# Kernel optimization log

Measured on AMD Instinct MI355X. Metric: run time of the kernel, lower is better.

## Reference

```python
import jax, jax.numpy as jnp
import numpy as np
from jax import lax

T, B, S, D, V = 128, 512, 128, 128, 50257


def setup_inputs() -> dict:
    key = jax.random.key(0)
    ks = jax.random.split(key, 6)
    words = jax.random.randint(ks[0], (T, B), 0, V, dtype=jnp.int64)
    masks = jnp.ones((T, B), dtype=jnp.float32)
    tparams = jax.random.normal(ks[1], (S, S), dtype=jnp.float32)
    tag_embed = jax.random.normal(ks[2], (S, D), dtype=jnp.float32)
    word_embed = jax.random.normal(ks[3], (V, D), dtype=jnp.float32)
    transform = jax.random.normal(ks[4], (D, D), dtype=jnp.float32) * 0.05 + jnp.eye(D, dtype=jnp.float32)
    correction = jax.random.normal(ks[5], (S, V), dtype=jnp.float32) * 0.05
    return {"words": words, "masks": masks, "tparams": tparams,
            "tag_embed": tag_embed, "word_embed": word_embed,
            "transform": transform, "correction": correction}


def reference(words, masks, tparams, tag_embed, word_embed, transform, correction):
    num_state = tparams.shape[0]
    # update_emission (unsupervised mode): project word embeddings, score against tags,
    # add correction, log_softmax over the vocab dimension (dim=0 of (V,S)).
    word_emb = word_embed @ transform                      # (V, D)
    log_emission = jax.nn.log_softmax(word_emb @ tag_embed.T + correction.T, axis=0)  # (V, S)
    # _calc_logA: log-normalized transition matrix (rows = source state)
    logA = jax.nn.log_softmax(tparams, axis=1)             # (S, S)
    # uniform log prior pi = log(1/S)
    log_pi = jnp.full((num_state,), jnp.log(1.0 / num_state), dtype=log_emission.dtype)

    em = log_emission[words]                               # (T, B, S) gathered densities

    alpha0 = log_pi[None, :] + em[0]                       # (B, S)

    def step(alpha, inp):
        dens, m = inp                                      # (B,S), (B,)
        # _forward_cell: logsumexp over previous state of alpha + logA + density
        new = jax.nn.logsumexp(alpha[:, :, None] + logA[None, :, :] + dens[:, None, :], axis=1)
        m = m[:, None]
        alpha = m * new + (1.0 - m) * alpha
        return alpha, None

    alpha, _ = lax.scan(step, alpha0, (em[1:], masks[1:]))
    objective = jnp.sum(jax.nn.logsumexp(alpha, axis=1))
    return -objective
```

## Files before the change

kernel.cpp:

```cpp
#include <hip/hip_runtime.h>
#include <math.h>

#define T_ 128
#define B_ 512
#define S_ 128
#define D_ 128
#define V_ 50257

#define K2_VT 64
#define K2_NB ((V_ + K2_VT - 1) / K2_VT)

__global__ __launch_bounds__(128) void k1_m2(const float* __restrict__ transform,
                                             const float* __restrict__ tag_embed,
                                             float* __restrict__ M2) {
  __shared__ float te[128][129];
  int tid = threadIdx.x;
  for (int r = 0; r < 128; ++r) te[r][tid] = tag_embed[r * 128 + tid];
  __syncthreads();
  int k = blockIdx.x;
  float acc = 0.f;
  #pragma unroll 8
  for (int d = 0; d < 128; ++d) acc += transform[k * 128 + d] * te[tid][d];
  M2[k * 128 + tid] = acc;
}

__global__ __launch_bounds__(64) void k1b_a(const float* __restrict__ tparams,
                                            float* __restrict__ A) {
  int i = blockIdx.x;
  int l = threadIdx.x;
  float x0 = tparams[i * 128 + l];
  float x1 = tparams[i * 128 + 64 + l];
  float m = fmaxf(x0, x1);
  #pragma unroll
  for (int off = 32; off; off >>= 1) m = fmaxf(m, __shfl_xor(m, off));
  float e0 = __expf(x0 - m), e1 = __expf(x1 - m);
  float s = e0 + e1;
  #pragma unroll
  for (int off = 32; off; off >>= 1) s += __shfl_xor(s, off);
  float inv = 1.f / s;
  A[i * 128 + l]      = e0 * inv;
  A[i * 128 + 64 + l] = e1 * inv;
}

__global__ __launch_bounds__(256, 2) void k2_logits(const float* __restrict__ we,
                                                 const float* __restrict__ M2,
                                                 const float* __restrict__ corr,
                                                 float* __restrict__ logits,
                                                 float* __restrict__ pmaxb,
                                                 float* __restrict__ psumb) {
  int tid = threadIdx.x;
  int sc = tid & 31;
  int vg = tid >> 5;
  long v0 = (long)blockIdx.x * K2_VT;
  __shared__ float weT[128][68];
  __shared__ float m2t[64][128];

  #pragma unroll
  for (int it = 0; it < 32; ++it) {
    int idx = it * 256 + tid;
    int d = idx & 127;
    int vv = idx >> 7;
    long v = v0 + vv;
    weT[d][vv] = (v < V_) ? we[v * 128 + d] : 0.f;
  }

  float acc[8][4];
  #pragma unroll
  for (int u = 0; u < 8; ++u)
    #pragma unroll
    for (int e = 0; e < 4; ++e) acc[u][e] = 0.f;

  #pragma unroll
  for (int c = 0; c < 2; ++c) {
    __syncthreads();
    #pragma unroll
    for (int it = 0; it < 32; ++it) {
      int idx = it * 256 + tid;
      int kr = idx >> 7, s = idx & 127;
      m2t[kr][s] = M2[(c * 64 + kr) * 128 + s];
    }
    __syncthreads();
    #pragma unroll 8
    for (int k = 0; k < 64; ++k) {
      float4 mv = *(const float4*)&m2t[k][4 * sc];
      float4 w0 = *(const float4*)&weT[c * 64 + k][8 * vg];
      float4 w1 = *(const float4*)&weT[c * 64 + k][8 * vg + 4];
      acc[0][0] += w0.x * mv.x; acc[0][1] += w0.x * mv.y; acc[0][2] += w0.x * mv.z; acc[0][3] += w0.x * mv.w;
      acc[1][0] += w0.y * mv.x; acc[1][1] += w0.y * mv.y; acc[1][2] += w0.y * mv.z; acc[1][3] += w0.y * mv.w;
      acc[2][0] += w0.z * mv.x; acc[2][1] += w0.z * mv.y; acc[2][2] += w0.z * mv.z; acc[2][3] += w0.z * mv.w;
      acc[3][0] += w0.w * mv.x; acc[3][1] += w0.w * mv.y; acc[3][2] += w0.w * mv.z; acc[3][3] += w0.w * mv.w;
      acc[4][0] += w1.x * mv.x; acc[4][1] += w1.x * mv.y; acc[4][2] += w1.x * mv.z; acc[4][3] += w1.x * mv.w;
      acc[5][0] += w1.y * mv.x; acc[5][1] += w1.y * mv.y; acc[5][2] += w1.y * mv.z; acc[5][3] += w1.y * mv.w;
      acc[6][0] += w1.z * mv.x; acc[6][1] += w1.z * mv.y; acc[6][2] += w1.z * mv.z; acc[6][3] += w1.z * mv.w;
      acc[7][0] += w1.w * mv.x; acc[7][1] += w1.w * mv.y; acc[7][2] += w1.w * mv.z; acc[7][3] += w1.w * mv.w;
    }
  }

  float lm[4], ls[4], Lst[8][4];
  #pragma unroll
  for (int e = 0; e < 4; ++e) { lm[e] = -INFINITY; ls[e] = 0.f; }
  long vbase = v0 + 8 * vg;
  #pragma unroll
  for (int e = 0; e < 4; ++e) {
    long rbase = (long)(4 * sc + e) * V_ + vbase;
    #pragma unroll
    for (int u = 0; u < 8; ++u) {
      if (vbase + u < V_) {
        float L = acc[u][e] + corr[rbase + u];
        Lst[u][e] = L;
        float nm = fmaxf(lm[e], L);
        ls[e] = ls[e] * __expf(lm[e] - nm) + __expf(L - nm);
        lm[e] = nm;
      }
    }
  }
  #pragma unroll
  for (int u = 0; u < 8; ++u) {
    long v = vbase + u;
    if (v < V_) {
      float4 st = make_float4(Lst[u][0], Lst[u][1], Lst[u][2], Lst[u][3]);
      *(float4*)&logits[v * 128 + 4 * sc] = st;
    }
  }

  __syncthreads();
  float* pmx = (float*)m2t;
  float* psm = pmx + 8 * 128;
  #pragma unroll
  for (int e = 0; e < 4; ++e) {
    pmx[vg * 128 + 4 * sc + e] = lm[e];
    psm[vg * 128 + 4 * sc + e] = ls[e];
  }
  __syncthreads();
  if (tid < 128) {
    int s = tid;
    float m = -INFINITY, sum = 0.f;
    #pragma unroll
    for (int g = 0; g < 8; ++g) {
      float pm = pmx[g * 128 + s];
      if (pm > -1e30f) {
        float ps = psm[g * 128 + s];
        float nm = fmaxf(m, pm);
        sum = sum * __expf(m - nm) + ps * __expf(pm - nm);
        m = nm;
      }
    }
    pmaxb[blockIdx.x * 128 + s] = m;
    psumb[blockIdx.x * 128 + s] = sum;
  }
}

__global__ __launch_bounds__(256) void k3_c(const float* __restrict__ pmaxb,
                                            const float* __restrict__ psumb,
                                            float* __restrict__ C) {
  int s = blockIdx.x;
  int t = threadIdx.x;
  float m = -INFINITY, sum = 0.f;
  #pragma unroll
  for (int q = 0; q < 4; ++q) {
    int b = t + q * 256;
    if (b < K2_NB) {
      float pm = pmaxb[b * 128 + s];
      if (pm > -1e30f) {
        float ps = psumb[b * 128 + s];
        float nm = fmaxf(m, pm);
        sum = sum * __expf(m - nm) + ps * __expf(pm - nm);
        m = nm;
      }
    }
  }
  #pragma unroll
  for (int off = 32; off; off >>= 1) {
    float om = __shfl_xor(m, off);
    float os = __shfl_xor(sum, off);
    float nm = fmaxf(m, om);
    sum = sum * __expf(m - nm) + os * __expf(om - nm);
    m = nm;
  }
  __shared__ float wm[4], wsv[4];
  int lane = t & 63, wv = t >> 6;
  if (lane == 0) { wm[wv] = m; wsv[wv] = sum; }
  __syncthreads();
  if (t == 0) {
    float M = fmaxf(fmaxf(wm[0], wm[1]), fmaxf(wm[2], wm[3]));
    float S = wsv[0] * __expf(wm[0] - M) + wsv[1] * __expf(wm[1] - M)
            + wsv[2] * __expf(wm[2] - M) + wsv[3] * __expf(wm[3] - M);
    C[s] = M + __logf(S);
  }
}

__global__ __launch_bounds__(512, 4) void k4_rec(const int* __restrict__ words,
                                              const float* __restrict__ masks,
                                              const float* __restrict__ A,
                                              const float* __restrict__ C,
                                              const float* __restrict__ logits,
                                              float* __restrict__ bv) {
  const float kB = 70.70101247f;
  int tid = threadIdx.x;
  int j = tid & 127;
  int h = tid >> 7;
  int b = blockIdx.x;
  int lane = tid & 63, w = tid >> 6;
  __shared__ __align__(16) float els[128];
  __shared__ __align__(16) float part[128][4];
  __shared__ __align__(16) float pmax4[4];
  __shared__ float wred[2];
  __shared__ int   wbuf[128];
  __shared__ float mbuf[128];
  if (tid < 128) {
    wbuf[j] = words[j * B_ + b];
    mbuf[j] = masks[j * B_ + b];
  }
  float Ac[32];
  #pragma unroll
  for (int k = 0; k < 32; ++k) Ac[k] = A[(h * 32 + k) * 128 + j];
  __syncthreads();

  float a = 0.f, S = 0.f, em_cur = 0.f, Lnext = 0.f, Cj = 0.f, a0 = 0.f;
  if (tid < 128) {
    Cj = C[j];
    a0 = -4.852030263919617f + logits[(unsigned)(wbuf[0] * 128 + j)] - Cj;
    float wm = a0;
    #pragma unroll
    for (int off = 32; off; off >>= 1) wm = fmaxf(wm, __shfl_xor(wm, off));
    if (lane == 0) wred[w] = wm;
  }
  __syncthreads();
  if (tid < 128) {
    float M0 = fmaxf(wred[0], wred[1]);
    a = __expf(a0 - M0);
    S = M0;
    els[j] = a;
    float L1 = logits[(unsigned)(wbuf[1] * 128 + j)];
    Lnext    = logits[(unsigned)(wbuf[2] * 128 + j)];
    em_cur = __expf(L1 - Cj + kB);
  }
  __syncthreads();

  for (int t = 1; t < T_; ++t) {
    float4 e0 = ((const float4*)els)[h * 8 + 0];
    float4 e1 = ((const float4*)els)[h * 8 + 1];
    float4 e2 = ((const float4*)els)[h * 8 + 2];
    float4 e3 = ((const float4*)els)[h * 8 + 3];
    float4 e4 = ((const float4*)els)[h * 8 + 4];
    float4 e5 = ((const float4*)els)[h * 8 + 5];
    float4 e6 = ((const float4*)els)[h * 8 + 6];
    float4 e7 = ((const float4*)els)[h * 8 + 7];
    float p0 = e0.x * Ac[0]  + e0.y * Ac[1]  + e0.z * Ac[2]  + e0.w * Ac[3]
             + e1.x * Ac[4]  + e1.y * Ac[5]  + e1.z * Ac[6]  + e1.w * Ac[7];
    float p1 = e2.x * Ac[8]  + e2.y * Ac[9]  + e2.z * Ac[10] + e2.w * Ac[11]
             + e3.x * Ac[12] + e3.y * Ac[13] + e3.z * Ac[14] + e3.w * Ac[15];
    float p2 = e4.x * Ac[16] + e4.y * Ac[17] + e4.z * Ac[18] + e4.w * Ac[19]
             + e5.x * Ac[20] + e5.y * Ac[21] + e5.z * Ac[22] + e5.w * Ac[23];
    float p3 = e6.x * Ac[24] + e6.y * Ac[25] + e6.z * Ac[26] + e6.w * Ac[27]
             + e7.x * Ac[28] + e7.y * Ac[29] + e7.z * Ac[30] + e7.w * Ac[31];
    part[j][h] = (p0 + p1) + (p2 + p3);
    if (j == 0) {
      float4 ma = make_float4(fmaxf(e0.x, e1.x), fmaxf(e0.y, e1.y), fmaxf(e0.z, e1.z), fmaxf(e0.w, e1.w));
      float4 mb = make_float4(fmaxf(e2.x, e3.x), fmaxf(e2.y, e3.y), fmaxf(e2.z, e3.z), fmaxf(e2.w, e3.w));
      float4 mc = make_float4(fmaxf(e4.x, e5.x), fmaxf(e4.y, e5.y), fmaxf(e4.z, e5.z), fmaxf(e4.w, e5.w));
      float4 md = make_float4(fmaxf(e6.x, e7.x), fmaxf(e6.y, e7.y), fmaxf(e6.z, e7.z), fmaxf(e6.w, e7.w));
      float4 m1 = make_float4(fmaxf(ma.x, mb.x), fmaxf(ma.y, mb.y), fmaxf(ma.z, mb.z), fmaxf(ma.w, mb.w));
      float4 m2 = make_float4(fmaxf(mc.x, md.x), fmaxf(mc.y, md.y), fmaxf(mc.z, md.z), fmaxf(mc.w, md.w));
      float mx = fmaxf(fmaxf(fmaxf(m1.x, m1.y), fmaxf(m1.z, m1.w)),
                       fmaxf(fmaxf(m2.x, m2.y), fmaxf(m2.z, m2.w)));
      pmax4[h] = mx;
    }
    float em_next = 0.f, Lf = 0.f;
    if (tid < 128) {
      if (t + 2 < T_) Lf = logits[(unsigned)(wbuf[t + 2] * 128 + j)];
      em_next = __expf(Lnext - Cj + kB);
    }
    __syncthreads();
    if (tid < 128) {
      float4 pm4 = *(const float4*)pmax4;
      float Mst = fmaxf(fmaxf(pm4.x, pm4.y), fmaxf(pm4.z, pm4.w));
      float invM = 1.f / Mst;
      float4 pp = *(const float4*)&part[j][0];
      float P = (pp.x + pp.y) + (pp.z + pp.w);
      float nv   = (P * invM) * em_cur;
      float oldq = (a * invM) * 0x1p102f;
      float mm = mbuf[t];
      a = mm * nv + (1.f - mm) * oldq;
      els[j] = a;
      S += __logf(Mst) - kB;
      em_cur = em_next;
      Lnext = Lf;
    }
    __syncthreads();
  }

  if (tid < 128) {
    float ss = a;
    #pragma unroll
    for (int off = 32; off; off >>= 1) ss += __shfl_xor(ss, off);
    if (lane == 0) wred[w] = ss;
  }
  __syncthreads();
  if (tid == 0) bv[b] = S + __logf(wred[0] + wred[1]);
}

__global__ __launch_bounds__(256) void k5_sum(const float* __restrict__ bv,
                                              float* __restrict__ out) {
  int t = threadIdx.x;
  float s = bv[t] + bv[t + 256];
  #pragma unroll
  for (int off = 32; off; off >>= 1) s += __shfl_xor(s, off);
  __shared__ float wsm[4];
  if ((t & 63) == 0) wsm[t >> 6] = s;
  __syncthreads();
  if (t == 0) out[0] = -(wsm[0] + wsm[1] + wsm[2] + wsm[3]);
}

extern "C" void kernel_launch(void* const* d_in, const int* in_sizes, int n_in,
                              void* d_out, int out_size, void* d_ws, size_t ws_size,
                              hipStream_t stream) {
  const int*   words      = (const int*)d_in[0];
  const float* masks      = (const float*)d_in[1];
  const float* tparams    = (const float*)d_in[2];
  const float* tag_embed  = (const float*)d_in[3];
  const float* word_embed = (const float*)d_in[4];
  const float* transform  = (const float*)d_in[5];
  const float* correction = (const float*)d_in[6];

  float* ws     = (float*)d_ws;
  float* M2     = ws;
  float* A      = ws + 16384;
  float* C      = ws + 32768;
  float* bv     = ws + 32896;
  float* pmaxb  = ws + 33408;
  float* psumb  = ws + 134016;
  float* logits = ws + 234624;

  hipLaunchKernelGGL(k1_m2,    dim3(128),    dim3(128), 0, stream, transform, tag_embed, M2);
  hipLaunchKernelGGL(k1b_a,    dim3(128),    dim3(64),  0, stream, tparams, A);
  hipLaunchKernelGGL(k2_logits,dim3(K2_NB),  dim3(256), 0, stream, word_embed, M2, correction, logits, pmaxb, psumb);
  hipLaunchKernelGGL(k3_c,     dim3(S_),     dim3(256), 0, stream, pmaxb, psumb, C);
  hipLaunchKernelGGL(k4_rec,   dim3(512),    dim3(512), 0, stream, words, masks, A, C, logits, bv);
  hipLaunchKernelGGL(k5_sum,   dim3(1),      dim3(256), 0, stream, bv, (float*)d_out);
}
```

Before: 193.4 us.

## Run recurrence with one wavefront per batch, holding full transition matrix in registers

The forward recurrence kernel now uses a single 64-lane wavefront per batch element instead of 512 threads. Each lane owns two states and keeps their full 128-entry columns of the transition matrix in registers. The per-step dot products, max and sum reductions are done with in-wave shuffles, so both block-wide barriers per time step go away. The cost is roughly eight times more FMAs per lane per step, very heavy register pressure with a possible spill, and only about two waves per CU to hide latency.

```diff
diff --git a/kernel.cpp b/kernel.cpp
--- a/kernel.cpp
+++ b/kernel.cpp
@@ -189,115 +189,112 @@
   }
 }
 
-__global__ __launch_bounds__(512, 4) void k4_rec(const int* __restrict__ words,
-                                              const float* __restrict__ masks,
-                                              const float* __restrict__ A,
-                                              const float* __restrict__ C,
-                                              const float* __restrict__ logits,
-                                              float* __restrict__ bv) {
+#define CHAIN8(EA, EB, AC, B) \
+  (EA.x * AC[B] + EA.y * AC[(B)+1] + EA.z * AC[(B)+2] + EA.w * AC[(B)+3] + \
+   EB.x * AC[(B)+4] + EB.y * AC[(B)+5] + EB.z * AC[(B)+6] + EB.w * AC[(B)+7])
+
+#define DOT_H(H, G0, G1) { \
+  float4 x0 = ELS4[(H)*8+0]; float4 x1 = ELS4[(H)*8+1]; \
+  float4 x2 = ELS4[(H)*8+2]; float4 x3 = ELS4[(H)*8+3]; \
+  float4 x4 = ELS4[(H)*8+4]; float4 x5 = ELS4[(H)*8+5]; \
+  float4 x6 = ELS4[(H)*8+6]; float4 x7 = ELS4[(H)*8+7]; \
+  float p00 = CHAIN8(x0, x1, Ac0, (H)*32+0); \
+  float p01 = CHAIN8(x2, x3, Ac0, (H)*32+8); \
+  float p02 = CHAIN8(x4, x5, Ac0, (H)*32+16); \
+  float p03 = CHAIN8(x6, x7, Ac0, (H)*32+24); \
+  float p10 = CHAIN8(x0, x1, Ac1, (H)*32+0); \
+  float p11 = CHAIN8(x2, x3, Ac1, (H)*32+8); \
+  float p12 = CHAIN8(x4, x5, Ac1, (H)*32+16); \
+  float p13 = CHAIN8(x6, x7, Ac1, (H)*32+24); \
+  G0 = (p00 + p01) + (p02 + p03); \
+  G1 = (p10 + p11) + (p12 + p13); }
+
+__global__ __launch_bounds__(64, 1) void k4_rec(const int* __restrict__ words,
+                                                const float* __restrict__ masks,
+                                                const float* __restrict__ A,
+                                                const float* __restrict__ C,
+                                                const float* __restrict__ logits,
+                                                float* __restrict__ bv) {
   const float kB = 70.70101247f;
-  int tid = threadIdx.x;
-  int j = tid & 127;
-  int h = tid >> 7;
+  int l = threadIdx.x;
   int b = blockIdx.x;
-  int lane = tid & 63, w = tid >> 6;
   __shared__ __align__(16) float els[128];
-  __shared__ __align__(16) float part[128][4];
-  __shared__ __align__(16) float pmax4[4];
-  __shared__ float wred[2];
   __shared__ int   wbuf[128];
   __shared__ float mbuf[128];
-  if (tid < 128) {
-    wbuf[j] = words[j * B_ + b];
-    mbuf[j] = masks[j * B_ + b];
-  }
-  float Ac[32];
-  #pragma unroll
-  for (int k = 0; k < 32; ++k) Ac[k] = A[(h * 32 + k) * 128 + j];
-  __syncthreads();
-
-  float a = 0.f, S = 0.f, em_cur = 0.f, Lnext = 0.f, Cj = 0.f, a0 = 0.f;
-  if (tid < 128) {
-    Cj = C[j];
-    a0 = -4.852030263919617f + logits[(unsigned)(wbuf[0] * 128 + j)] - Cj;
-    float wm = a0;
-    #pragma unroll
-    for (int off = 32; off; off >>= 1) wm = fmaxf(wm, __shfl_xor(wm, off));
-    if (lane == 0) wred[w] = wm;
-  }
-  __syncthreads();
-  if (tid < 128) {
-    float M0 = fmaxf(wred[0], wred[1]);
-    a = __expf(a0 - M0);
-    S = M0;
-    els[j] = a;
-    float L1 = logits[(unsigned)(wbuf[1] * 128 + j)];
-    Lnext    = logits[(unsigned)(wbuf[2] * 128 + j)];
-    em_cur = __expf(L1 - Cj + kB);
-  }
-  __syncthreads();
+  wbuf[l]      = words[l * B_ + b];
+  wbuf[l + 64] = words[(l + 64) * B_ + b];
+  mbuf[l]      = masks[l * B_ + b];
+  mbuf[l + 64] = masks[(l + 64) * B_ + b];
+
+  float Ac0[128], Ac1[128];
+  #pragma unroll
+  for (int i = 0; i < 128; ++i) {
+    Ac0[i] = A[i * 128 + l];
+    Ac1[i] = A[i * 128 + 64 + l];
+  }
+  float Cj0 = C[l], Cj1 = C[l + 64];
+  __syncthreads();
+
+  int w0 = wbuf[0];
+  float a0i = -4.852030263919617f + logits[(unsigned)(w0 * 128 + l)] - Cj0;
+  float a1i = -4.852030263919617f + logits[(unsigned)(w0 * 128 + 64 + l)] - Cj1;
+  float m0 = a0i, m1 = a1i;
+  #pragma unroll
+  for (int off = 32; off; off >>= 1) {
+    m0 = fmaxf(m0, __shfl_xor(m0, off));
+    m1 = fmaxf(m1, __shfl_xor(m1, off));
+  }
+  float M0 = fmaxf(m0, m1);
+  float a0 = __expf(a0i - M0), a1 = __expf(a1i - M0);
+  float S = M0;
+  els[l] = a0; els[l + 64] = a1;
+  float Mst = fmaxf(a0, a1);
+  #pragma unroll
+  for (int off = 32; off; off >>= 1) Mst = fmaxf(Mst, __shfl_xor(Mst, off));
+  int w1 = wbuf[1];
+  float Lc0 = logits[(unsigned)(w1 * 128 + l)];
+  float Lc1 = logits[(unsigned)(w1 * 128 + 64 + l)];
+
+  const float4* ELS4 = (const float4*)els;
 
   for (int t = 1; t < T_; ++t) {
-    float4 e0 = ((const float4*)els)[h * 8 + 0];
-    float4 e1 = ((const float4*)els)[h * 8 + 1];
-    float4 e2 = ((const float4*)els)[h * 8 + 2];
-    float4 e3 = ((const float4*)els)[h * 8 + 3];
-    float4 e4 = ((const float4*)els)[h * 8 + 4];
-    float4 e5 = ((const float4*)els)[h * 8 + 5];
-    float4 e6 = ((const float4*)els)[h * 8 + 6];
-    float4 e7 = ((const float4*)els)[h * 8 + 7];
-    float p0 = e0.x * Ac[0]  + e0.y * Ac[1]  + e0.z * Ac[2]  + e0.w * Ac[3]
-             + e1.x * Ac[4]  + e1.y * Ac[5]  + e1.z * Ac[6]  + e1.w * Ac[7];
-    float p1 = e2.x * Ac[8]  + e2.y * Ac[9]  + e2.z * Ac[10] + e2.w * Ac[11]
-             + e3.x * Ac[12] + e3.y * Ac[13] + e3.z * Ac[14] + e3.w * Ac[15];
-    float p2 = e4.x * Ac[16] + e4.y * Ac[17] + e4.z * Ac[18] + e4.w * Ac[19]
-             + e5.x * Ac[20] + e5.y * Ac[21] + e5.z * Ac[22] + e5.w * Ac[23];
-    float p3 = e6.x * Ac[24] + e6.y * Ac[25] + e6.z * Ac[26] + e6.w * Ac[27]
-             + e7.x * Ac[28] + e7.y * Ac[29] + e7.z * Ac[30] + e7.w * Ac[31];
-    part[j][h] = (p0 + p1) + (p2 + p3);
-    if (j == 0) {
-      float4 ma = make_float4(fmaxf(e0.x, e1.x), fmaxf(e0.y, e1.y), fmaxf(e0.z, e1.z), fmaxf(e0.w, e1.w));
-      float4 mb = make_float4(fmaxf(e2.x, e3.x), fmaxf(e2.y, e3.y), fmaxf(e2.z, e3.z), fmaxf(e2.w, e3.w));
-      float4 mc = make_float4(fmaxf(e4.x, e5.x), fmaxf(e4.y, e5.y), fmaxf(e4.z, e5.z), fmaxf(e4.w, e5.w));
-      float4 md = make_float4(fmaxf(e6.x, e7.x), fmaxf(e6.y, e7.y), fmaxf(e6.z, e7.z), fmaxf(e6.w, e7.w));
-      float4 m1 = make_float4(fmaxf(ma.x, mb.x), fmaxf(ma.y, mb.y), fmaxf(ma.z, mb.z), fmaxf(ma.w, mb.w));
-      float4 m2 = make_float4(fmaxf(mc.x, md.x), fmaxf(mc.y, md.y), fmaxf(mc.z, md.z), fmaxf(mc.w, md.w));
-      float mx = fmaxf(fmaxf(fmaxf(m1.x, m1.y), fmaxf(m1.z, m1.w)),
-                       fmaxf(fmaxf(m2.x, m2.y), fmaxf(m2.z, m2.w)));
-      pmax4[h] = mx;
-    }
-    float em_next = 0.f, Lf = 0.f;
-    if (tid < 128) {
-      if (t + 2 < T_) Lf = logits[(unsigned)(wbuf[t + 2] * 128 + j)];
-      em_next = __expf(Lnext - Cj + kB);
-    }
-    __syncthreads();
-    if (tid < 128) {
-      float4 pm4 = *(const float4*)pmax4;
-      float Mst = fmaxf(fmaxf(pm4.x, pm4.y), fmaxf(pm4.z, pm4.w));
-      float invM = 1.f / Mst;
-      float4 pp = *(const float4*)&part[j][0];
-      float P = (pp.x + pp.y) + (pp.z + pp.w);
-      float nv   = (P * invM) * em_cur;
-      float oldq = (a * invM) * 0x1p102f;
-      float mm = mbuf[t];
-      a = mm * nv + (1.f - mm) * oldq;
-      els[j] = a;
-      S += __logf(Mst) - kB;
-      em_cur = em_next;
-      Lnext = Lf;
-    }
-    __syncthreads();
-  }
-
-  if (tid < 128) {
-    float ss = a;
-    #pragma unroll
-    for (int off = 32; off; off >>= 1) ss += __shfl_xor(ss, off);
-    if (lane == 0) wred[w] = ss;
-  }
-  __syncthreads();
-  if (tid == 0) bv[b] = S + __logf(wred[0] + wred[1]);
+    int wn = wbuf[(t < T_ - 1) ? (t + 1) : t];
+    float Lp0 = logits[(unsigned)(wn * 128 + l)];
+    float Lp1 = logits[(unsigned)(wn * 128 + 64 + l)];
+
+    float G00, G01, G02, G03, G10, G11, G12, G13;
+    DOT_H(0, G00, G10)
+    DOT_H(1, G01, G11)
+    DOT_H(2, G02, G12)
+    DOT_H(3, G03, G13)
+    float P0 = (G00 + G01) + (G02 + G03);
+    float P1 = (G10 + G11) + (G12 + G13);
+
+    float em0 = __expf(Lc0 - Cj0 + kB);
+    float em1 = __expf(Lc1 - Cj1 + kB);
+    float invM = 1.f / Mst;
+    float mm = mbuf[t];
+    float nv0 = (P0 * invM) * em0;
+    float nv1 = (P1 * invM) * em1;
+    float oldq0 = (a0 * invM) * 0x1p102f;
+    float oldq1 = (a1 * invM) * 0x1p102f;
+    a0 = mm * nv0 + (1.f - mm) * oldq0;
+    a1 = mm * nv1 + (1.f - mm) * oldq1;
+    els[l] = a0; els[l + 64] = a1;
+    S += __logf(Mst) - kB;
+    Mst = fmaxf(a0, a1);
+    #pragma unroll
+    for (int off = 32; off; off >>= 1) Mst = fmaxf(Mst, __shfl_xor(Mst, off));
+    Lc0 = Lp0; Lc1 = Lp1;
+  }
+
+  float s0 = a0, s1 = a1;
+  #pragma unroll
+  for (int off = 32; off; off >>= 1) {
+    s0 += __shfl_xor(s0, off);
+    s1 += __shfl_xor(s1, off);
+  }
+  if (l == 0) bv[b] = S + __logf(s0 + s1);
 }
 
 __global__ __launch_bounds__(256) void k5_sum(const float* __restrict__ bv,
@@ -336,6 +333,6 @@
   hipLaunchKernelGGL(k1b_a,    dim3(128),    dim3(64),  0, stream, tparams, A);
   hipLaunchKernelGGL(k2_logits,dim3(K2_NB),  dim3(256), 0, stream, word_embed, M2, correction, logits, pmaxb, psumb);
   hipLaunchKernelGGL(k3_c,     dim3(S_),     dim3(256), 0, stream, pmaxb, psumb, C);
-  hipLaunchKernelGGL(k4_rec,   dim3(512),    dim3(512), 0, stream, words, masks, A, C, logits, bv);
+  hipLaunchKernelGGL(k4_rec,   dim3(512),    dim3(64),  0, stream, words, masks, A, C, logits, bv);
   hipLaunchKernelGGL(k5_sum,   dim3(1),      dim3(256), 0, stream, bv, (float*)d_out);
 }
```

New measurement: 210.0 us. 8.6% more time.

## Process two batch sequences per block in forward recurrence to reuse transition registers

Applied to the files above, without the earlier changes.

The forward-recurrence kernel now handles two batch elements per block instead of one. Each thread applies its 32 register-resident transition coefficients to both sequences' alpha vectors, and twice as many threads take part in the elementwise update. The grid halves to 256 blocks, which spreads the per-step barrier and A-load cost over more work. In exchange register pressure rises (launch bounds lowered to 2 blocks per CU) and fewer blocks are in flight across the device.

```diff
diff --git a/kernel.cpp b/kernel.cpp
--- a/kernel.cpp
+++ b/kernel.cpp
@@ -189,100 +189,116 @@
   }
 }
 
-__global__ __launch_bounds__(512, 4) void k4_rec(const int* __restrict__ words,
-                                              const float* __restrict__ masks,
-                                              const float* __restrict__ A,
-                                              const float* __restrict__ C,
-                                              const float* __restrict__ logits,
-                                              float* __restrict__ bv) {
+#define CHAIN8(EA, EB, AC, BASE) \
+  (EA.x * AC[(BASE)]   + EA.y * AC[(BASE)+1] + EA.z * AC[(BASE)+2] + EA.w * AC[(BASE)+3] + \
+   EB.x * AC[(BASE)+4] + EB.y * AC[(BASE)+5] + EB.z * AC[(BASE)+6] + EB.w * AC[(BASE)+7])
+
+#define SLICEMAX8(E0,E1,E2,E3,E4,E5,E6,E7, OUT) { \
+  float4 ma = make_float4(fmaxf(E0.x,E1.x), fmaxf(E0.y,E1.y), fmaxf(E0.z,E1.z), fmaxf(E0.w,E1.w)); \
+  float4 mb = make_float4(fmaxf(E2.x,E3.x), fmaxf(E2.y,E3.y), fmaxf(E2.z,E3.z), fmaxf(E2.w,E3.w)); \
+  float4 mc = make_float4(fmaxf(E4.x,E5.x), fmaxf(E4.y,E5.y), fmaxf(E4.z,E5.z), fmaxf(E4.w,E5.w)); \
+  float4 md = make_float4(fmaxf(E6.x,E7.x), fmaxf(E6.y,E7.y), fmaxf(E6.z,E7.z), fmaxf(E6.w,E7.w)); \
+  float4 m1 = make_float4(fmaxf(ma.x,mb.x), fmaxf(ma.y,mb.y), fmaxf(ma.z,mb.z), fmaxf(ma.w,mb.w)); \
+  float4 m2 = make_float4(fmaxf(mc.x,md.x), fmaxf(mc.y,md.y), fmaxf(mc.z,md.z), fmaxf(mc.w,md.w)); \
+  OUT = fmaxf(fmaxf(fmaxf(m1.x,m1.y), fmaxf(m1.z,m1.w)), \
+              fmaxf(fmaxf(m2.x,m2.y), fmaxf(m2.z,m2.w))); }
+
+__global__ __launch_bounds__(512, 2) void k4_rec(const int* __restrict__ words,
+                                                 const float* __restrict__ masks,
+                                                 const float* __restrict__ A,
+                                                 const float* __restrict__ C,
+                                                 const float* __restrict__ logits,
+                                                 float* __restrict__ bv) {
   const float kB = 70.70101247f;
   int tid = threadIdx.x;
   int j = tid & 127;
   int h = tid >> 7;
-  int b = blockIdx.x;
-  int lane = tid & 63, w = tid >> 6;
-  __shared__ __align__(16) float els[128];
-  __shared__ __align__(16) float part[128][4];
-  __shared__ __align__(16) float pmax4[4];
-  __shared__ float wred[2];
-  __shared__ int   wbuf[128];
-  __shared__ float mbuf[128];
-  if (tid < 128) {
-    wbuf[j] = words[j * B_ + b];
-    mbuf[j] = masks[j * B_ + b];
+  int b0 = blockIdx.x * 2;
+  int lane = tid & 63;
+  __shared__ __align__(16) float els[2][128];
+  __shared__ float part[2][4][128];
+  __shared__ __align__(16) float pmax[2][4];
+  __shared__ float sred[2][2];
+  __shared__ int   wbuf[2][128];
+  __shared__ float mbuf[2][128];
+
+  if (tid < 256) {
+    int gg = tid >> 7, t0 = tid & 127;
+    wbuf[gg][t0] = words[t0 * B_ + b0 + gg];
+    mbuf[gg][t0] = masks[t0 * B_ + b0 + gg];
   }
   float Ac[32];
   #pragma unroll
   for (int k = 0; k < 32; ++k) Ac[k] = A[(h * 32 + k) * 128 + j];
   __syncthreads();
 
-  float a = 0.f, S = 0.f, em_cur = 0.f, Lnext = 0.f, Cj = 0.f, a0 = 0.f;
-  if (tid < 128) {
+  int g = (tid >> 7) & 1;
+  float a = 0.f, S = 0.f, em_cur = 0.f, Lnext = 0.f, Cj = 0.f, a0i = 0.f;
+  if (tid < 256) {
     Cj = C[j];
-    a0 = -4.852030263919617f + logits[(unsigned)(wbuf[0] * 128 + j)] - Cj;
-    float wm = a0;
+    a0i = -4.852030263919617f + logits[(unsigned)(wbuf[g][0] * 128 + j)] - Cj;
+    float wm = a0i;
     #pragma unroll
     for (int off = 32; off; off >>= 1) wm = fmaxf(wm, __shfl_xor(wm, off));
-    if (lane == 0) wred[w] = wm;
-  }
-  __syncthreads();
-  if (tid < 128) {
-    float M0 = fmaxf(wred[0], wred[1]);
-    a = __expf(a0 - M0);
+    if (lane == 0) sred[g][(tid >> 6) & 1] = wm;
+  }
+  __syncthreads();
+  if (tid < 256) {
+    float M0 = fmaxf(sred[g][0], sred[g][1]);
+    a = __expf(a0i - M0);
     S = M0;
-    els[j] = a;
-    float L1 = logits[(unsigned)(wbuf[1] * 128 + j)];
-    Lnext    = logits[(unsigned)(wbuf[2] * 128 + j)];
+    els[g][j] = a;
+    float L1 = logits[(unsigned)(wbuf[g][1] * 128 + j)];
+    Lnext    = logits[(unsigned)(wbuf[g][2] * 128 + j)];
     em_cur = __expf(L1 - Cj + kB);
   }
   __syncthreads();
 
+  const float4* E0 = (const float4*)&els[0][0];
+  const float4* E1 = (const float4*)&els[1][0];
+
   for (int t = 1; t < T_; ++t) {
-    float4 e0 = ((const float4*)els)[h * 8 + 0];
-    float4 e1 = ((const float4*)els)[h * 8 + 1];
-    float4 e2 = ((const float4*)els)[h * 8 + 2];
-    float4 e3 = ((const float4*)els)[h * 8 + 3];
-    float4 e4 = ((const float4*)els)[h * 8 + 4];
-    float4 e5 = ((const float4*)els)[h * 8 + 5];
-    float4 e6 = ((const float4*)els)[h * 8 + 6];
-    float4 e7 = ((const float4*)els)[h * 8 + 7];
-    float p0 = e0.x * Ac[0]  + e0.y * Ac[1]  + e0.z * Ac[2]  + e0.w * Ac[3]
-             + e1.x * Ac[4]  + e1.y * Ac[5]  + e1.z * Ac[6]  + e1.w * Ac[7];
-    float p1 = e2.x * Ac[8]  + e2.y * Ac[9]  + e2.z * Ac[10] + e2.w * Ac[11]
-             + e3.x * Ac[12] + e3.y * Ac[13] + e3.z * Ac[14] + e3.w * Ac[15];
-    float p2 = e4.x * Ac[16] + e4.y * Ac[17] + e4.z * Ac[18] + e4.w * Ac[19]
-             + e5.x * Ac[20] + e5.y * Ac[21] + e5.z * Ac[22] + e5.w * Ac[23];
-    float p3 = e6.x * Ac[24] + e6.y * Ac[25] + e6.z * Ac[26] + e6.w * Ac[27]
-             + e7.x * Ac[28] + e7.y * Ac[29] + e7.z * Ac[30] + e7.w * Ac[31];
-    part[j][h] = (p0 + p1) + (p2 + p3);
+    float4 x0 = E0[h * 8 + 0], x1 = E0[h * 8 + 1], x2 = E0[h * 8 + 2], x3 = E0[h * 8 + 3];
+    float4 x4 = E0[h * 8 + 4], x5 = E0[h * 8 + 5], x6 = E0[h * 8 + 6], x7 = E0[h * 8 + 7];
+    float4 y0 = E1[h * 8 + 0], y1 = E1[h * 8 + 1], y2 = E1[h * 8 + 2], y3 = E1[h * 8 + 3];
+    float4 y4 = E1[h * 8 + 4], y5 = E1[h * 8 + 5], y6 = E1[h * 8 + 6], y7 = E1[h * 8 + 7];
+    {
+      float p0 = CHAIN8(x0, x1, Ac, 0);
+      float p1 = CHAIN8(x2, x3, Ac, 8);
+      float p2 = CHAIN8(x4, x5, Ac, 16);
+      float p3 = CHAIN8(x6, x7, Ac, 24);
+      part[0][h][j] = (p0 + p1) + (p2 + p3);
+    }
+    {
+      float p0 = CHAIN8(y0, y1, Ac, 0);
+      float p1 = CHAIN8(y2, y3, Ac, 8);
+      float p2 = CHAIN8(y4, y5, Ac, 16);
+      float p3 = CHAIN8(y6, y7, Ac, 24);
+      part[1][h][j] = (p0 + p1) + (p2 + p3);
+    }
     if (j == 0) {
-      float4 ma = make_float4(fmaxf(e0.x, e1.x), fmaxf(e0.y, e1.y), fmaxf(e0.z, e1.z), fmaxf(e0.w, e1.w));
-      float4 mb = make_float4(fmaxf(e2.x, e3.x), fmaxf(e2.y, e3.y), fmaxf(e2.z, e3.z), fmaxf(e2.w, e3.w));
-      float4 mc = make_float4(fmaxf(e4.x, e5.x), fmaxf(e4.y, e5.y), fmaxf(e4.z, e5.z), fmaxf(e4.w, e5.w));
-      float4 md = make_float4(fmaxf(e6.x, e7.x), fmaxf(e6.y, e7.y), fmaxf(e6.z, e7.z), fmaxf(e6.w, e7.w));
-      float4 m1 = make_float4(fmaxf(ma.x, mb.x), fmaxf(ma.y, mb.y), fmaxf(ma.z, mb.z), fmaxf(ma.w, mb.w));
-      float4 m2 = make_float4(fmaxf(mc.x, md.x), fmaxf(mc.y, md.y), fmaxf(mc.z, md.z), fmaxf(mc.w, md.w));
-      float mx = fmaxf(fmaxf(fmaxf(m1.x, m1.y), fmaxf(m1.z, m1.w)),
-                       fmaxf(fmaxf(m2.x, m2.y), fmaxf(m2.z, m2.w)));
-      pmax4[h] = mx;
+      float mx0, mx1;
+      SLICEMAX8(x0, x1, x2, x3, x4, x5, x6, x7, mx0)
+      SLICEMAX8(y0, y1, y2, y3, y4, y5, y6, y7, mx1)
+      pmax[0][h] = mx0;
+      pmax[1][h] = mx1;
     }
     float em_next = 0.f, Lf = 0.f;
-    if (tid < 128) {
-      if (t + 2 < T_) Lf = logits[(unsigned)(wbuf[t + 2] * 128 + j)];
+    if (tid < 256) {
+      if (t + 2 < T_) Lf = logits[(unsigned)(wbuf[g][t + 2] * 128 + j)];
       em_next = __expf(Lnext - Cj + kB);
     }
     __syncthreads();
-    if (tid < 128) {
-      float4 pm4 = *(const float4*)pmax4;
+    if (tid < 256) {
+      float4 pm4 = *(const float4*)pmax[g];
       float Mst = fmaxf(fmaxf(pm4.x, pm4.y), fmaxf(pm4.z, pm4.w));
       float invM = 1.f / Mst;
-      float4 pp = *(const float4*)&part[j][0];
-      float P = (pp.x + pp.y) + (pp.z + pp.w);
+      float P = (part[g][0][j] + part[g][1][j]) + (part[g][2][j] + part[g][3][j]);
       float nv   = (P * invM) * em_cur;
       float oldq = (a * invM) * 0x1p102f;
-      float mm = mbuf[t];
+      float mm = mbuf[g][t];
       a = mm * nv + (1.f - mm) * oldq;
-      els[j] = a;
+      els[g][j] = a;
       S += __logf(Mst) - kB;
       em_cur = em_next;
       Lnext = Lf;
@@ -290,14 +306,15 @@
     __syncthreads();
   }
 
-  if (tid < 128) {
+  if (tid < 256) {
     float ss = a;
     #pragma unroll
     for (int off = 32; off; off >>= 1) ss += __shfl_xor(ss, off);
-    if (lane == 0) wred[w] = ss;
-  }
-  __syncthreads();
-  if (tid == 0) bv[b] = S + __logf(wred[0] + wred[1]);
+    if (lane == 0) sred[g][(tid >> 6) & 1] = ss;
+  }
+  __syncthreads();
+  if (tid == 0)   bv[b0]     = S + __logf(sred[0][0] + sred[0][1]);
+  if (tid == 128) bv[b0 + 1] = S + __logf(sred[1][0] + sred[1][1]);
 }
 
 __global__ __launch_bounds__(256) void k5_sum(const float* __restrict__ bv,
@@ -336,6 +353,6 @@
   hipLaunchKernelGGL(k1b_a,    dim3(128),    dim3(64),  0, stream, tparams, A);
   hipLaunchKernelGGL(k2_logits,dim3(K2_NB),  dim3(256), 0, stream, word_embed, M2, correction, logits, pmaxb, psumb);
   hipLaunchKernelGGL(k3_c,     dim3(S_),     dim3(256), 0, stream, pmaxb, psumb, C);
-  hipLaunchKernelGGL(k4_rec,   dim3(512),    dim3(512), 0, stream, words, masks, A, C, logits, bv);
+  hipLaunchKernelGGL(k4_rec,   dim3(256),    dim3(512), 0, stream, words, masks, A, C, logits, bv);
   hipLaunchKernelGGL(k5_sum,   dim3(1),      dim3(256), 0, stream, bv, (float*)d_out);
 }
```

New measurement: 194.6 us. About the same (+0.6%).

## Stream word embeddings directly from global in logits GEMM, transpose partial-sum buffer

Applied to the files above, without the earlier changes.

The logits kernel no longer stages a transposed word-embedding tile in shared memory. Each thread now loads its eight embedding rows straight from global memory as float4 per k-chunk. This frees shared memory, so the occupancy hint rises from 2 to 4 blocks per CU, and the M2 tile is loaded with float4 copies. In the recurrence kernel the partial-sum buffer becomes [4][128] to avoid strided LDS writes, at the cost of four scalar reads instead of one float4 read.

```diff
diff --git a/kernel.cpp b/kernel.cpp
--- a/kernel.cpp
+++ b/kernel.cpp
@@ -42,7 +42,18 @@
   A[i * 128 + 64 + l] = e1 * inv;
 }
 
-__global__ __launch_bounds__(256, 2) void k2_logits(const float* __restrict__ we,
+#define K2STEP(COMP, KK) { \
+  float4 mv = *(const float4*)&m2t[(KK)][4 * sc]; \
+  acc[0][0] += wr[0].COMP * mv.x; acc[0][1] += wr[0].COMP * mv.y; acc[0][2] += wr[0].COMP * mv.z; acc[0][3] += wr[0].COMP * mv.w; \
+  acc[1][0] += wr[1].COMP * mv.x; acc[1][1] += wr[1].COMP * mv.y; acc[1][2] += wr[1].COMP * mv.z; acc[1][3] += wr[1].COMP * mv.w; \
+  acc[2][0] += wr[2].COMP * mv.x; acc[2][1] += wr[2].COMP * mv.y; acc[2][2] += wr[2].COMP * mv.z; acc[2][3] += wr[2].COMP * mv.w; \
+  acc[3][0] += wr[3].COMP * mv.x; acc[3][1] += wr[3].COMP * mv.y; acc[3][2] += wr[3].COMP * mv.z; acc[3][3] += wr[3].COMP * mv.w; \
+  acc[4][0] += wr[4].COMP * mv.x; acc[4][1] += wr[4].COMP * mv.y; acc[4][2] += wr[4].COMP * mv.z; acc[4][3] += wr[4].COMP * mv.w; \
+  acc[5][0] += wr[5].COMP * mv.x; acc[5][1] += wr[5].COMP * mv.y; acc[5][2] += wr[5].COMP * mv.z; acc[5][3] += wr[5].COMP * mv.w; \
+  acc[6][0] += wr[6].COMP * mv.x; acc[6][1] += wr[6].COMP * mv.y; acc[6][2] += wr[6].COMP * mv.z; acc[6][3] += wr[6].COMP * mv.w; \
+  acc[7][0] += wr[7].COMP * mv.x; acc[7][1] += wr[7].COMP * mv.y; acc[7][2] += wr[7].COMP * mv.z; acc[7][3] += wr[7].COMP * mv.w; }
+
+__global__ __launch_bounds__(256, 4) void k2_logits(const float* __restrict__ we,
                                                  const float* __restrict__ M2,
                                                  const float* __restrict__ corr,
                                                  float* __restrict__ logits,
@@ -51,17 +62,14 @@
   int tid = threadIdx.x;
   int sc = tid & 31;
   int vg = tid >> 5;
-  long v0 = (long)blockIdx.x * K2_VT;
-  __shared__ float weT[128][68];
+  unsigned v0 = (unsigned)blockIdx.x * K2_VT;
   __shared__ float m2t[64][128];
 
-  #pragma unroll
-  for (int it = 0; it < 32; ++it) {
-    int idx = it * 256 + tid;
-    int d = idx & 127;
-    int vv = idx >> 7;
-    long v = v0 + vv;
-    weT[d][vv] = (v < V_) ? we[v * 128 + d] : 0.f;
+  unsigned vrow[8];
+  #pragma unroll
+  for (int u = 0; u < 8; ++u) {
+    unsigned v = v0 + 8 * vg + u;
+    vrow[u] = (v < V_ ? v : (V_ - 1)) * 128u;
   }
 
   float acc[8][4];
@@ -74,32 +82,30 @@
   for (int c = 0; c < 2; ++c) {
     __syncthreads();
     #pragma unroll
-    for (int it = 0; it < 32; ++it) {
+    for (int it = 0; it < 8; ++it) {
       int idx = it * 256 + tid;
-      int kr = idx >> 7, s = idx & 127;
-      m2t[kr][s] = M2[(c * 64 + kr) * 128 + s];
+      int kr = idx >> 5;
+      int scol = (idx & 31) * 4;
+      *(float4*)&m2t[kr][scol] = *(const float4*)&M2[(c * 64 + kr) * 128 + scol];
     }
     __syncthreads();
-    #pragma unroll 8
-    for (int k = 0; k < 64; ++k) {
-      float4 mv = *(const float4*)&m2t[k][4 * sc];
-      float4 w0 = *(const float4*)&weT[c * 64 + k][8 * vg];
-      float4 w1 = *(const float4*)&weT[c * 64 + k][8 * vg + 4];
-      acc[0][0] += w0.x * mv.x; acc[0][1] += w0.x * mv.y; acc[0][2] += w0.x * mv.z; acc[0][3] += w0.x * mv.w;
-      acc[1][0] += w0.y * mv.x; acc[1][1] += w0.y * mv.y; acc[1][2] += w0.y * mv.z; acc[1][3] += w0.y * mv.w;
-      acc[2][0] += w0.z * mv.x; acc[2][1] += w0.z * mv.y; acc[2][2] += w0.z * mv.z; acc[2][3] += w0.z * mv.w;
-      acc[3][0] += w0.w * mv.x; acc[3][1] += w0.w * mv.y; acc[3][2] += w0.w * mv.z; acc[3][3] += w0.w * mv.w;
-      acc[4][0] += w1.x * mv.x; acc[4][1] += w1.x * mv.y; acc[4][2] += w1.x * mv.z; acc[4][3] += w1.x * mv.w;
-      acc[5][0] += w1.y * mv.x; acc[5][1] += w1.y * mv.y; acc[5][2] += w1.y * mv.z; acc[5][3] += w1.y * mv.w;
-      acc[6][0] += w1.z * mv.x; acc[6][1] += w1.z * mv.y; acc[6][2] += w1.z * mv.z; acc[6][3] += w1.z * mv.w;
-      acc[7][0] += w1.w * mv.x; acc[7][1] += w1.w * mv.y; acc[7][2] += w1.w * mv.z; acc[7][3] += w1.w * mv.w;
+    #pragma unroll 4
+    for (int kc = 0; kc < 64; kc += 4) {
+      float4 wr[8];
+      #pragma unroll
+      for (int u = 0; u < 8; ++u)
+        wr[u] = *(const float4*)&we[vrow[u] + (unsigned)(c * 64 + kc)];
+      K2STEP(x, kc + 0)
+      K2STEP(y, kc + 1)
+      K2STEP(z, kc + 2)
+      K2STEP(w, kc + 3)
     }
   }
 
   float lm[4], ls[4], Lst[8][4];
   #pragma unroll
   for (int e = 0; e < 4; ++e) { lm[e] = -INFINITY; ls[e] = 0.f; }
-  long vbase = v0 + 8 * vg;
+  long vbase = (long)v0 + 8 * vg;
   #pragma unroll
   for (int e = 0; e < 4; ++e) {
     long rbase = (long)(4 * sc + e) * V_ + vbase;
@@ -202,7 +208,7 @@
   int b = blockIdx.x;
   int lane = tid & 63, w = tid >> 6;
   __shared__ __align__(16) float els[128];
-  __shared__ __align__(16) float part[128][4];
+  __shared__ float part[4][128];
   __shared__ __align__(16) float pmax4[4];
   __shared__ float wred[2];
   __shared__ int   wbuf[128];
@@ -254,7 +260,7 @@
              + e5.x * Ac[20] + e5.y * Ac[21] + e5.z * Ac[22] + e5.w * Ac[23];
     float p3 = e6.x * Ac[24] + e6.y * Ac[25] + e6.z * Ac[26] + e6.w * Ac[27]
              + e7.x * Ac[28] + e7.y * Ac[29] + e7.z * Ac[30] + e7.w * Ac[31];
-    part[j][h] = (p0 + p1) + (p2 + p3);
+    part[h][j] = (p0 + p1) + (p2 + p3);
     if (j == 0) {
       float4 ma = make_float4(fmaxf(e0.x, e1.x), fmaxf(e0.y, e1.y), fmaxf(e0.z, e1.z), fmaxf(e0.w, e1.w));
       float4 mb = make_float4(fmaxf(e2.x, e3.x), fmaxf(e2.y, e3.y), fmaxf(e2.z, e3.z), fmaxf(e2.w, e3.w));
@@ -276,8 +282,7 @@
       float4 pm4 = *(const float4*)pmax4;
       float Mst = fmaxf(fmaxf(pm4.x, pm4.y), fmaxf(pm4.z, pm4.w));
       float invM = 1.f / Mst;
-      float4 pp = *(const float4*)&part[j][0];
-      float P = (pp.x + pp.y) + (pp.z + pp.w);
+      float P = (part[0][j] + part[1][j]) + (part[2][j] + part[3][j]);
       float nv   = (P * invM) * em_cur;
       float oldq = (a * invM) * 0x1p102f;
       float mm = mbuf[t];
```

After: 192.5 us. No clear change (-0.5%).
